# Kernel tuning notes

Measured on AMD Instinct MI355X. Metric: run time of the kernel, lower is better.

## Reference

```python
import jax, jax.numpy as jnp
import numpy as np

B, H, N, P = 2, 8, 2048, 64   # batch, heads, seq, head_dim
M, D = 4, 256                 # sketch count, sketch feature dim


def setup_inputs() -> dict:
    key = jax.random.key(0)
    kq, kk, ks, kr = jax.random.split(key, 4)
    scale = P ** -0.5  # keep exp(QK) numerically tame, std(dot) ~= 1/8
    Q = jax.random.normal(kq, (B, H, N, P), dtype=jnp.float32) * scale
    K = jax.random.normal(kk, (B, H, N, P), dtype=jnp.float32) * scale
    # indices into the concatenated [Q;K] token axis of length 2N
    sketching_matrix = jax.random.randint(ks, (B, M, D), 0, 2 * N)
    # Rademacher random signs, broadcast over [b,h,2n] in the reduction
    random_sign = jnp.sign(jax.random.normal(kr, (M, D), dtype=jnp.float32))
    random_sign = jnp.where(random_sign == 0, 1.0, random_sign)
    return {"Q": Q, "K": K, "sketching_matrix": sketching_matrix,
            "random_sign": random_sign}


def reference(Q, K, sketching_matrix, random_sign):
    b, h, n, p = Q.shape
    X = jnp.concatenate([Q, K], axis=2)          # [b,h,2n,p]
    Xt = jnp.transpose(X, (0, 2, 1, 3))          # [b,2n,h,p]
    # gather sketched landmarks: [b,m,d,h,p] -> [b,h,m,d,p]
    XS = Xt[jnp.arange(b)[:, None, None], sketching_matrix]
    XS = jnp.transpose(XS, (0, 3, 1, 2, 4))
    # RS_SM accumulate branch: exp of inner products, random-sign reduce over m
    product = jnp.einsum('bhnp,bhmdp->bhnmd', X, XS)   # [b,h,2n,m,d]
    AS = jnp.einsum('bhnmd,md->bhnd', jnp.exp(product), random_sign)
    return AS.astype(Q.dtype)                    # [b,h,2n,d]
```

## Files before the change

kernel.cpp:

```cpp
#include <hip/hip_runtime.h>
#include <hip/hip_bf16.h>

typedef __attribute__((ext_vector_type(8))) short short8;
typedef __attribute__((ext_vector_type(4))) float f32x4;

namespace {
constexpr int Nc  = 2048;
constexpr int NXc = 4096;
constexpr int Pc  = 64;
constexpr int Mc  = 4;
constexpr int Dc  = 256;
constexpr int BH  = 16;
constexpr int NCHUNK = 128;
constexpr int NT = NCHUNK / 16;
constexpr float LOG2E = 1.4426950408889634f;
}

__device__ inline float fexp2(float x) {
#if __has_builtin(__builtin_amdgcn_exp2f)
  return __builtin_amdgcn_exp2f(x);
#else
  return exp2f(x);
#endif
}

__device__ inline unsigned int bfpack(float a, float b) {
  union { __hip_bfloat162 h; unsigned int u; } cv;
  cv.h = __float22bfloat162_rn(make_float2(a, b));
  return cv.u;
}

__global__ __launch_bounds__(256) void prepass_kernel(
    const float* __restrict__ Q, const float* __restrict__ K,
    const int* __restrict__ SK, __hip_bfloat16* __restrict__ Wb)
{
  const int t  = blockIdx.x * 256 + threadIdx.x;
  const int q  = t & 7;
  const int r  = t >> 3;
  const int bh = r >> 10;
  const int md = r & 1023;
  const int b  = bh >> 3;
  const int idx = SK[b * (Mc * Dc) + md];
  const float* src = (idx < Nc) ? (Q + ((size_t)bh * Nc + idx) * Pc)
                                : (K + ((size_t)bh * Nc + (idx - Nc)) * Pc);
  const f32x4* s4 = (const f32x4*)(src + q * 8);
  f32x4 f0 = s4[0], f1 = s4[1];
  uint4 u;
  u.x = bfpack(f0.x * LOG2E, f0.y * LOG2E);
  u.y = bfpack(f0.z * LOG2E, f0.w * LOG2E);
  u.z = bfpack(f1.x * LOG2E, f1.y * LOG2E);
  u.w = bfpack(f1.z * LOG2E, f1.w * LOG2E);
  *(uint4*)(Wb + (size_t)r * Pc + q * 8) = u;
}

__global__ __launch_bounds__(256, 2) void sketch_main(
    const float* __restrict__ Q, const float* __restrict__ K,
    const __hip_bfloat16* __restrict__ Wb,
    const float* __restrict__ SGN, float* __restrict__ OUT)
{
  const int t    = threadIdx.x;
  const int lane = t & 63;
  const int wv   = t >> 6;
  const int brow = lane & 15;
  const int q    = lane >> 4;
  const int bh   = blockIdx.y;
  const int n0   = blockIdx.x * NCHUNK;

  short8 wf[4][4][2];
  {
    const __hip_bfloat16* wbase =
        Wb + ((size_t)bh * (Mc * Dc) + wv * 64 + brow) * Pc + q * 8;
    #pragma unroll
    for (int m = 0; m < 4; ++m) {
      #pragma unroll
      for (int dt = 0; dt < 4; ++dt) {
        const __hip_bfloat16* wp = wbase + (size_t)(m * Dc + dt * 16) * Pc;
        wf[m][dt][0] = *(const short8*)(wp);
        wf[m][dt][1] = *(const short8*)(wp + 32);
      }
    }
  }

  f32x4 sg[4][4];
  #pragma unroll
  for (int m = 0; m < 4; ++m) {
    #pragma unroll
    for (int dt = 0; dt < 4; ++dt) {
      sg[m][dt] = *(const f32x4*)(SGN + m * Dc + wv * 64 + dt * 16 + q * 4);
    }
  }

  const float* xrow = ((n0 < Nc) ? (Q + ((size_t)bh * Nc + n0) * Pc)
                                 : (K + ((size_t)bh * Nc + (n0 - Nc)) * Pc))
                      + (size_t)brow * Pc + q * 8;
  float* obase = OUT + ((size_t)bh * NXc + n0 + brow) * Dc + wv * 64 + q * 4;

  f32x4 xa = *(const f32x4*)(xrow);
  f32x4 xb = *(const f32x4*)(xrow + 4);
  f32x4 xc = *(const f32x4*)(xrow + 32);
  f32x4 xd = *(const f32x4*)(xrow + 36);

  for (int it = 0; it < NT; ++it) {
    short8 b0, b1;
    {
      union { short8 s; uint4 u; } c0, c1;
      c0.u.x = bfpack(xa.x, xa.y); c0.u.y = bfpack(xa.z, xa.w);
      c0.u.z = bfpack(xb.x, xb.y); c0.u.w = bfpack(xb.z, xb.w);
      c1.u.x = bfpack(xc.x, xc.y); c1.u.y = bfpack(xc.z, xc.w);
      c1.u.z = bfpack(xd.x, xd.y); c1.u.w = bfpack(xd.z, xd.w);
      b0 = c0.s; b1 = c1.s;
    }
    if (it + 1 < NT) {
      const float* xn = xrow + (size_t)(it + 1) * 16 * Pc;
      xa = *(const f32x4*)(xn);
      xb = *(const f32x4*)(xn + 4);
      xc = *(const f32x4*)(xn + 32);
      xd = *(const f32x4*)(xn + 36);
    }

    float* orow = obase + (size_t)it * 16 * Dc;
    #pragma unroll
    for (int dt = 0; dt < 4; ++dt) {
      f32x4 acc = {0.f, 0.f, 0.f, 0.f};
      #pragma unroll
      for (int m = 0; m < 4; ++m) {
        f32x4 c = {0.f, 0.f, 0.f, 0.f};
        c = __builtin_amdgcn_mfma_f32_16x16x32_bf16(wf[m][dt][0], b0, c, 0, 0, 0);
        c = __builtin_amdgcn_mfma_f32_16x16x32_bf16(wf[m][dt][1], b1, c, 0, 0, 0);
        const f32x4 s = sg[m][dt];
        acc.x = fmaf(s.x, fexp2(c.x), acc.x);
        acc.y = fmaf(s.y, fexp2(c.y), acc.y);
        acc.z = fmaf(s.z, fexp2(c.z), acc.z);
        acc.w = fmaf(s.w, fexp2(c.w), acc.w);
      }
      *(f32x4*)(orow + dt * 16) = acc;
    }
  }
}

extern "C" void kernel_launch(void* const* d_in, const int* in_sizes, int n_in,
                              void* d_out, int out_size, void* d_ws, size_t ws_size,
                              hipStream_t stream) {
  (void)in_sizes; (void)n_in; (void)out_size; (void)ws_size;
  const float* Q   = (const float*)d_in[0];
  const float* K   = (const float*)d_in[1];
  const int*   SK  = (const int*)d_in[2];
  const float* SGN = (const float*)d_in[3];
  float* OUT = (float*)d_out;

  __hip_bfloat16* Wb = (__hip_bfloat16*)d_ws;

  prepass_kernel<<<dim3(512), dim3(256), 0, stream>>>(Q, K, SK, Wb);
  sketch_main<<<dim3(NXc / NCHUNK, BH), dim3(256), 0, stream>>>(Q, K, Wb, SGN, OUT);
}
```

Before: 111.0 us.

## Split D across blocks, hold X tile in registers, remap blocks per XCD

The main kernel now splits the 256-wide sketch dimension into four 64-column slices per block, with each wave owning 16 columns. The 128-row X tile is held in registers as bf16 fragments and the weight fragments are streamed per m. This lowers register pressure, allowing launch bounds of 3 blocks per SM, and the grid grows from 32 to 128 blocks per head. Block indices are remapped so the blocks sharing an X chunk land on the same XCD for L2 reuse, at the cost of each X tile being loaded and converted four times.

```diff
diff --git a/kernel.cpp b/kernel.cpp
--- a/kernel.cpp
+++ b/kernel.cpp
@@ -11,8 +11,6 @@
 constexpr int Mc  = 4;
 constexpr int Dc  = 256;
 constexpr int BH  = 16;
-constexpr int NCHUNK = 128;
-constexpr int NT = NCHUNK / 16;
 constexpr float LOG2E = 1.4426950408889634f;
 }
 
@@ -53,7 +51,7 @@
   *(uint4*)(Wb + (size_t)r * Pc + q * 8) = u;
 }
 
-__global__ __launch_bounds__(256, 2) void sketch_main(
+__global__ __launch_bounds__(256, 3) void sketch_main(
     const float* __restrict__ Q, const float* __restrict__ K,
     const __hip_bfloat16* __restrict__ Wb,
     const float* __restrict__ SGN, float* __restrict__ OUT)
@@ -64,77 +62,62 @@
   const int brow = lane & 15;
   const int q    = lane >> 4;
   const int bh   = blockIdx.y;
-  const int n0   = blockIdx.x * NCHUNK;
 
-  short8 wf[4][4][2];
-  {
-    const __hip_bfloat16* wbase =
-        Wb + ((size_t)bh * (Mc * Dc) + wv * 64 + brow) * Pc + q * 8;
+  const int bx  = blockIdx.x;
+  const int xcd = bx & 7;
+  const int rr  = bx >> 3;
+  const int nch = xcd * 4 + (rr >> 2);
+  const int dq  = rr & 3;
+  const int n0  = nch * 128;
+  const int dbase = dq * 64 + wv * 16;
+
+  const float* xbase = ((n0 < Nc) ? (Q + ((size_t)bh * Nc + n0) * Pc)
+                                  : (K + ((size_t)bh * Nc + (n0 - Nc)) * Pc))
+                       + (size_t)brow * Pc + q * 8;
+  short8 b0[8], b1[8];
+  #pragma unroll
+  for (int it = 0; it < 8; ++it) {
+    const float* xp = xbase + (size_t)it * 16 * Pc;
+    f32x4 xa = *(const f32x4*)(xp);
+    f32x4 xb = *(const f32x4*)(xp + 4);
+    f32x4 xc = *(const f32x4*)(xp + 32);
+    f32x4 xd = *(const f32x4*)(xp + 36);
+    union { short8 s; uint4 u; } c0, c1;
+    c0.u.x = bfpack(xa.x, xa.y); c0.u.y = bfpack(xa.z, xa.w);
+    c0.u.z = bfpack(xb.x, xb.y); c0.u.w = bfpack(xb.z, xb.w);
+    c1.u.x = bfpack(xc.x, xc.y); c1.u.y = bfpack(xc.z, xc.w);
+    c1.u.z = bfpack(xd.x, xd.y); c1.u.w = bfpack(xd.z, xd.w);
+    b0[it] = c0.s; b1[it] = c1.s;
+  }
+
+  f32x4 acc[8];
+  #pragma unroll
+  for (int it = 0; it < 8; ++it) acc[it] = (f32x4){0.f, 0.f, 0.f, 0.f};
+
+  const __hip_bfloat16* wq =
+      Wb + ((size_t)bh * (Mc * Dc) + dbase + brow) * Pc + q * 8;
+  #pragma unroll
+  for (int m = 0; m < 4; ++m) {
+    const __hip_bfloat16* wp = wq + (size_t)m * Dc * Pc;
+    short8 a0 = *(const short8*)(wp);
+    short8 a1 = *(const short8*)(wp + 32);
+    const f32x4 sg = *(const f32x4*)(SGN + m * Dc + dbase + q * 4);
     #pragma unroll
-    for (int m = 0; m < 4; ++m) {
-      #pragma unroll
-      for (int dt = 0; dt < 4; ++dt) {
-        const __hip_bfloat16* wp = wbase + (size_t)(m * Dc + dt * 16) * Pc;
-        wf[m][dt][0] = *(const short8*)(wp);
-        wf[m][dt][1] = *(const short8*)(wp + 32);
-      }
+    for (int it = 0; it < 8; ++it) {
+      f32x4 c = {0.f, 0.f, 0.f, 0.f};
+      c = __builtin_amdgcn_mfma_f32_16x16x32_bf16(a0, b0[it], c, 0, 0, 0);
+      c = __builtin_amdgcn_mfma_f32_16x16x32_bf16(a1, b1[it], c, 0, 0, 0);
+      acc[it].x = fmaf(sg.x, fexp2(c.x), acc[it].x);
+      acc[it].y = fmaf(sg.y, fexp2(c.y), acc[it].y);
+      acc[it].z = fmaf(sg.z, fexp2(c.z), acc[it].z);
+      acc[it].w = fmaf(sg.w, fexp2(c.w), acc[it].w);
     }
   }
 
-  f32x4 sg[4][4];
   #pragma unroll
-  for (int m = 0; m < 4; ++m) {
-    #pragma unroll
-    for (int dt = 0; dt < 4; ++dt) {
-      sg[m][dt] = *(const f32x4*)(SGN + m * Dc + wv * 64 + dt * 16 + q * 4);
-    }
-  }
-
-  const float* xrow = ((n0 < Nc) ? (Q + ((size_t)bh * Nc + n0) * Pc)
-                                 : (K + ((size_t)bh * Nc + (n0 - Nc)) * Pc))
-                      + (size_t)brow * Pc + q * 8;
-  float* obase = OUT + ((size_t)bh * NXc + n0 + brow) * Dc + wv * 64 + q * 4;
-
-  f32x4 xa = *(const f32x4*)(xrow);
-  f32x4 xb = *(const f32x4*)(xrow + 4);
-  f32x4 xc = *(const f32x4*)(xrow + 32);
-  f32x4 xd = *(const f32x4*)(xrow + 36);
-
-  for (int it = 0; it < NT; ++it) {
-    short8 b0, b1;
-    {
-      union { short8 s; uint4 u; } c0, c1;
-      c0.u.x = bfpack(xa.x, xa.y); c0.u.y = bfpack(xa.z, xa.w);
-      c0.u.z = bfpack(xb.x, xb.y); c0.u.w = bfpack(xb.z, xb.w);
-      c1.u.x = bfpack(xc.x, xc.y); c1.u.y = bfpack(xc.z, xc.w);
-      c1.u.z = bfpack(xd.x, xd.y); c1.u.w = bfpack(xd.z, xd.w);
-      b0 = c0.s; b1 = c1.s;
-    }
-    if (it + 1 < NT) {
-      const float* xn = xrow + (size_t)(it + 1) * 16 * Pc;
-      xa = *(const f32x4*)(xn);
-      xb = *(const f32x4*)(xn + 4);
-      xc = *(const f32x4*)(xn + 32);
-      xd = *(const f32x4*)(xn + 36);
-    }
-
-    float* orow = obase + (size_t)it * 16 * Dc;
-    #pragma unroll
-    for (int dt = 0; dt < 4; ++dt) {
-      f32x4 acc = {0.f, 0.f, 0.f, 0.f};
-      #pragma unroll
-      for (int m = 0; m < 4; ++m) {
-        f32x4 c = {0.f, 0.f, 0.f, 0.f};
-        c = __builtin_amdgcn_mfma_f32_16x16x32_bf16(wf[m][dt][0], b0, c, 0, 0, 0);
-        c = __builtin_amdgcn_mfma_f32_16x16x32_bf16(wf[m][dt][1], b1, c, 0, 0, 0);
-        const f32x4 s = sg[m][dt];
-        acc.x = fmaf(s.x, fexp2(c.x), acc.x);
-        acc.y = fmaf(s.y, fexp2(c.y), acc.y);
-        acc.z = fmaf(s.z, fexp2(c.z), acc.z);
-        acc.w = fmaf(s.w, fexp2(c.w), acc.w);
-      }
-      *(f32x4*)(orow + dt * 16) = acc;
-    }
+  for (int it = 0; it < 8; ++it) {
+    float* op = OUT + ((size_t)bh * NXc + n0 + it * 16 + brow) * Dc + dbase + q * 4;
+    *(f32x4*)op = acc[it];
   }
 }
 
@@ -151,5 +134,5 @@
   __hip_bfloat16* Wb = (__hip_bfloat16*)d_ws;
 
   prepass_kernel<<<dim3(512), dim3(256), 0, stream>>>(Q, K, SK, Wb);
-  sketch_main<<<dim3(NXc / NCHUNK, BH), dim3(256), 0, stream>>>(Q, K, Wb, SGN, OUT);
+  sketch_main<<<dim3(128, BH), dim3(256), 0, stream>>>(Q, K, Wb, SGN, OUT);
 }
```

Measured after the change: 137.6 us. +24.0%, slower.
